# Kernel tuning notes

Measured on AMD Instinct MI355X. Metric: run time of the kernel, lower is better.

Reference implementation:

```python
import jax, jax.numpy as jnp
import numpy as np

H, HD = 8, 32            # num_heads, head_dim
OUT = H * HD             # out_channels = 256
NUM_GRAPHS = 1


def segment_softmax(logits, seg, num_segments):
    m = jax.ops.segment_max(logits, seg, num_segments=num_segments)
    m = jnp.where(jnp.isfinite(m), m, 0.0)
    e = jnp.exp(logits - m[seg])
    s = jax.ops.segment_sum(e, seg, num_segments=num_segments)
    return e / (s[seg] + 1e-16)


def setup_inputs():
    key = jax.random.key(0)
    ks = jax.random.split(key, 16)
    N, E, IN = 30000, 600000, 128
    s = 0.05
    return {
        "x": jax.random.normal(ks[0], (N, IN), jnp.float32),
        "edge_index": jax.random.randint(ks[1], (2, E), 0, N, jnp.int32),
        "edge_attr": jax.random.normal(ks[2], (E,), jnp.float32),
        "batch": jnp.zeros((N,), jnp.int32),
        # per-head GATConv params (stacked over heads)
        "W": jax.random.normal(ks[3], (H, IN, HD), jnp.float32) * s,
        "a_src": jax.random.normal(ks[4], (H, HD), jnp.float32) * s,
        "a_dst": jax.random.normal(ks[5], (H, HD), jnp.float32) * s,
        "conv_b": jnp.zeros((H, HD), jnp.float32),
        # shared fc (used twice in forward)
        "fc_w": jax.random.normal(ks[6], (OUT, OUT), jnp.float32) * s,
        "fc_b": jnp.zeros((OUT,), jnp.float32),
        "ln_w": jnp.ones((OUT,), jnp.float32),
        "ln_b": jnp.zeros((OUT,), jnp.float32),
        "gate_w": jax.random.normal(ks[7], (1, OUT), jnp.float32) * s,
        "gate_b": jnp.zeros((1,), jnp.float32),
        "gfc_w": jax.random.normal(ks[8], (OUT, OUT), jnp.float32) * s,
        "gfc_b": jnp.zeros((OUT,), jnp.float32),
    }


def reference(x, edge_index, edge_attr, batch, W, a_src, a_dst, conv_b,
              fc_w, fc_b, ln_w, ln_b, gate_w, gate_b, gfc_w, gfc_b):
    N = x.shape[0]
    # (dropout p=0.2 is identity in eval mode)
    # --- multi-head GATConv (heads=1 each, vectorized over H); PyG default
    # add_self_loops=True; edge_dim=None so edge_attr is ignored by the conv.
    loops = jnp.arange(N, dtype=edge_index.dtype)
    src = jnp.concatenate([edge_index[0], loops])  # [Etot]
    dst = jnp.concatenate([edge_index[1], loops])
    xp = jnp.einsum('ni,hid->nhd', x, W)                    # [N,H,HD]
    alpha_src = jnp.sum(xp * a_src[None], axis=-1)          # [N,H]
    alpha_dst = jnp.sum(xp * a_dst[None], axis=-1)          # [N,H]
    logits = jax.nn.leaky_relu(alpha_src[src] + alpha_dst[dst], 0.2)  # [Etot,H]
    alpha = segment_softmax(logits, dst, N)                 # [Etot,H]
    msg = alpha[:, :, None] * xp[src]                        # [Etot,H,HD]
    out = jax.ops.segment_sum(msg, dst, num_segments=N) + conv_b[None]
    x_local = out.reshape(N, OUT)                            # concat over heads
    # --- dense re-attention / softmax fusion
    sa = jax.nn.softmax(jax.nn.leaky_relu(x_local @ fc_w.T + fc_b, 0.01), axis=-1)
    x_local = jax.nn.leaky_relu(x_local * sa, 0.2)
    x_local = x_local @ fc_w.T + fc_b
    # LayerNorm (eps=1e-5)
    mu = jnp.mean(x_local, axis=-1, keepdims=True)
    var = jnp.mean(jnp.square(x_local - mu), axis=-1, keepdims=True)
    x_local = (x_local - mu) / jnp.sqrt(var + 1e-5) * ln_w + ln_b
    # F.normalize(p=2, dim=1)
    nrm = jnp.sqrt(jnp.sum(jnp.square(x_local), axis=1, keepdims=True))
    x_local = x_local / jnp.maximum(nrm, 1e-12)
    # --- GlobalAttention pooling
    gate = (x_local @ gate_w.T + gate_b)[:, 0]               # [N]
    g = segment_softmax(gate, batch, NUM_GRAPHS)             # [N]
    x_global = jax.ops.segment_sum(g[:, None] * x_local, batch,
                                   num_segments=NUM_GRAPHS)  # [1,OUT]
    ga = jax.nn.softmax(jax.nn.relu(x_global @ gfc_w.T + gfc_b), axis=-1)
    return x_local * ga[batch]                               # [N,OUT]
```

## Files before the change

kernel.cpp:

```cpp
#include <hip/hip_runtime.h>


#define PAD 96

typedef __attribute__((ext_vector_type(8))) short bf16x8;
typedef __attribute__((ext_vector_type(4))) float f32x4;

__device__ __forceinline__ float leaky_f(float v, float s) { return v > 0.f ? v : s * v; }
__device__ __forceinline__ unsigned short f2bf(float f) {
  unsigned int u = __float_as_uint(f);
  u += 0x7fffu + ((u >> 16) & 1u);
  return (unsigned short)(u >> 16);
}
__device__ __forceinline__ float bf2f(unsigned short u) {
  return __uint_as_float(((unsigned int)u) << 16);
}
__device__ __forceinline__ float red16_sum(float v) {
#pragma unroll
  for (int m = 1; m < 16; m <<= 1) v += __shfl_xor(v, m);
  return v;
}
__device__ __forceinline__ float red16_max(float v) {
#pragma unroll
  for (int m = 1; m < 16; m <<= 1) v = fmaxf(v, __shfl_xor(v, m));
  return v;
}

__global__ void repack_zero_kernel(const float* __restrict__ W, const float* __restrict__ fc_w,
                                   const float* __restrict__ gfc_w,
                                   unsigned short* __restrict__ Wb,
                                   unsigned short* __restrict__ fcB, float* __restrict__ gfcT,
                                   int* __restrict__ count, float* __restrict__ xg,
                                   float* __restrict__ S, int* __restrict__ done, int n) {
  int i = blockIdx.x * 256 + threadIdx.x;
  if (i < 256 * 128) {
    int c = i >> 7, k = i & 127;
    Wb[i] = f2bf(W[((c >> 5) * 128 + k) * 32 + (c & 31)]);
  } else if (i < 256 * 128 + 256 * 256) {
    int j = i - 256 * 128;
    fcB[j] = f2bf(fc_w[j]);
  } else if (i < 256 * 128 + 2 * 256 * 256) {
    int j = i - 256 * 128 - 256 * 256;
    gfcT[j] = gfc_w[(j & 255) * 256 + (j >> 8)];
  }
  if (i < n) count[i] = 0;
  if (i < 256) xg[i] = 0.f;
  if (i == 0) { S[0] = 0.f; done[0] = 0; }
}

template <int A_BF16>
__device__ __forceinline__ void gemm_body_64x256(
    const void* __restrict__ Av, const unsigned short* __restrict__ B,
    int row0, int n_rows, int K, short As[64][72], short Bs[256][72],
    f32x4 acc[4][4]) {
  int t = threadIdx.x;
  int wave = t >> 6, lane = t & 63;
  int m16 = lane & 15, quad = lane >> 4;
  int wc = wave * 64;
  for (int k0 = 0; k0 < K; k0 += 64) {
    if (A_BF16) {
      const unsigned short* A = (const unsigned short*)Av;
#pragma unroll
      for (int p = 0; p < 2; ++p) {
        int e = (p * 256 + t) * 8;
        int row = e >> 6, k = e & 63;
        int ar = row0 + row; if (ar > n_rows - 1) ar = n_rows - 1;
        uint4 q = *(const uint4*)(A + (size_t)ar * K + k0 + k);
        *(uint4*)&As[row][k] = q;
      }
    } else {
      const float* A = (const float*)Av;
#pragma unroll
      for (int p = 0; p < 4; ++p) {
        int e = (p * 256 + t) * 4;
        int row = e >> 6, k = e & 63;
        int ar = row0 + row; if (ar > n_rows - 1) ar = n_rows - 1;
        float4 q = *(const float4*)(A + (size_t)ar * K + k0 + k);
        unsigned int lo = (unsigned int)f2bf(q.x) | ((unsigned int)f2bf(q.y) << 16);
        unsigned int hi = (unsigned int)f2bf(q.z) | ((unsigned int)f2bf(q.w) << 16);
        *(uint2*)&As[row][k] = make_uint2(lo, hi);
      }
    }
#pragma unroll
    for (int p = 0; p < 8; ++p) {
      int e = (p * 256 + t) * 8;
      int nn = e >> 6, k = e & 63;
      uint4 q = *(const uint4*)(B + (size_t)nn * K + k0 + k);
      *(uint4*)&Bs[nn][k] = q;
    }
    __syncthreads();
#pragma unroll
    for (int ks = 0; ks < 64; ks += 32) {
      bf16x8 af[4], bfr[4];
#pragma unroll
      for (int i = 0; i < 4; ++i)
        af[i] = *(const bf16x8*)&As[i * 16 + m16][ks + quad * 8];
#pragma unroll
      for (int j = 0; j < 4; ++j)
        bfr[j] = *(const bf16x8*)&Bs[wc + j * 16 + m16][ks + quad * 8];
#pragma unroll
      for (int i = 0; i < 4; ++i)
#pragma unroll
        for (int j = 0; j < 4; ++j)
          acc[i][j] = __builtin_amdgcn_mfma_f32_16x16x32_bf16(af[i], bfr[j], acc[i][j], 0, 0, 0);
    }
    __syncthreads();
  }
}

__global__ __launch_bounds__(256) void gemm_xp_scatter(
    const float* __restrict__ A, const unsigned short* __restrict__ B,
    const float* __restrict__ a_src, const float* __restrict__ a_dst,
    unsigned short* __restrict__ xpb, float* __restrict__ asrc,
    float* __restrict__ adst, int n_rows,
    const int* __restrict__ esrc, const int* __restrict__ edst,
    int* __restrict__ count, int* __restrict__ ssrc, int E, int gemm_blocks) {
  __shared__ short As[64][72];
  __shared__ short Bs[256][72];
  if ((int)blockIdx.x >= gemm_blocks) {
    int i = ((int)blockIdx.x - gemm_blocks) * 256 + threadIdx.x;
    if (i < E) {
      int d = edst[i];
      int p = atomicAdd(&count[d], 1);
      if (p < PAD) ssrc[(size_t)d * PAD + p] = esrc[i];
    }
    return;
  }
  int t = threadIdx.x;
  int wave = t >> 6, lane = t & 63;
  int m16 = lane & 15, quad = lane >> 4;
  int wc = wave * 64;
  int row0 = blockIdx.x * 64;
  f32x4 acc[4][4];
#pragma unroll
  for (int i = 0; i < 4; ++i)
#pragma unroll
    for (int j = 0; j < 4; ++j) acc[i][j] = (f32x4){0.f, 0.f, 0.f, 0.f};
  gemm_body_64x256<0>(A, B, row0, n_rows, 128, As, Bs, acc);

  float av[4], bd[4];
#pragma unroll
  for (int j = 0; j < 4; ++j) {
    int c = wc + j * 16 + m16;
    av[j] = a_src[c];
    bd[j] = a_dst[c];
  }
#pragma unroll
  for (int i = 0; i < 4; ++i)
#pragma unroll
    for (int v = 0; v < 4; ++v) {
      int r = row0 + i * 16 + quad * 4 + v;
      if (r < n_rows) {
#pragma unroll
        for (int j = 0; j < 4; ++j)
          xpb[(size_t)r * 256 + wc + j * 16 + m16] = f2bf(acc[i][j][v]);
      }
      float s0 = acc[i][0][v] * av[0] + acc[i][1][v] * av[1];
      float s1 = acc[i][2][v] * av[2] + acc[i][3][v] * av[3];
      float d0 = acc[i][0][v] * bd[0] + acc[i][1][v] * bd[1];
      float d1 = acc[i][2][v] * bd[2] + acc[i][3][v] * bd[3];
      s0 = red16_sum(s0); s1 = red16_sum(s1);
      d0 = red16_sum(d0); d1 = red16_sum(d1);
      if (m16 == 0 && r < n_rows) {
        asrc[(size_t)r * 8 + 2 * wave] = s0;
        asrc[(size_t)r * 8 + 2 * wave + 1] = s1;
        adst[(size_t)r * 8 + 2 * wave] = d0;
        adst[(size_t)r * 8 + 2 * wave + 1] = d1;
      }
    }
}

__global__ __launch_bounds__(256) void gemm_sm(
    const float* __restrict__ A, const unsigned short* __restrict__ B,
    const float* __restrict__ bias, unsigned short* __restrict__ x2b, int n_rows) {
  __shared__ short As[64][72];
  __shared__ short Bs[256][72];
  __shared__ float red[4][64];
  __shared__ float rowv[64];
  int t = threadIdx.x;
  int wave = t >> 6, lane = t & 63;
  int m16 = lane & 15, quad = lane >> 4;
  int wc = wave * 64;
  int row0 = blockIdx.x * 64;
  f32x4 acc[4][4];
#pragma unroll
  for (int i = 0; i < 4; ++i)
#pragma unroll
    for (int j = 0; j < 4; ++j) acc[i][j] = (f32x4){0.f, 0.f, 0.f, 0.f};
  gemm_body_64x256<0>(A, B, row0, n_rows, 256, As, Bs, acc);

  float bvv[4];
#pragma unroll
  for (int j = 0; j < 4; ++j) bvv[j] = bias[wc + j * 16 + m16];
#pragma unroll
  for (int i = 0; i < 4; ++i)
#pragma unroll
    for (int j = 0; j < 4; ++j)
#pragma unroll
      for (int v = 0; v < 4; ++v)
        acc[i][j][v] = leaky_f(acc[i][j][v] + bvv[j], 0.01f);

  float M[4][4];
#pragma unroll
  for (int i = 0; i < 4; ++i)
#pragma unroll
    for (int v = 0; v < 4; ++v) {
      float m = fmaxf(fmaxf(acc[i][0][v], acc[i][1][v]), fmaxf(acc[i][2][v], acc[i][3][v]));
      M[i][v] = red16_max(m);
    }
  if (m16 == 0)
#pragma unroll
    for (int i = 0; i < 4; ++i)
#pragma unroll
      for (int v = 0; v < 4; ++v) red[wave][i * 16 + quad * 4 + v] = M[i][v];
  __syncthreads();
  if (t < 64) rowv[t] = fmaxf(fmaxf(red[0][t], red[1][t]), fmaxf(red[2][t], red[3][t]));
  __syncthreads();
#pragma unroll
  for (int i = 0; i < 4; ++i)
#pragma unroll
    for (int v = 0; v < 4; ++v) M[i][v] = rowv[i * 16 + quad * 4 + v];
  __syncthreads();

  float S[4][4];
#pragma unroll
  for (int i = 0; i < 4; ++i)
#pragma unroll
    for (int v = 0; v < 4; ++v) {
#pragma unroll
      for (int j = 0; j < 4; ++j) acc[i][j][v] = __expf(acc[i][j][v] - M[i][v]);
      float s = acc[i][0][v] + acc[i][1][v] + acc[i][2][v] + acc[i][3][v];
      S[i][v] = red16_sum(s);
    }
  if (m16 == 0)
#pragma unroll
    for (int i = 0; i < 4; ++i)
#pragma unroll
      for (int v = 0; v < 4; ++v) red[wave][i * 16 + quad * 4 + v] = S[i][v];
  __syncthreads();
  if (t < 64) rowv[t] = red[0][t] + red[1][t] + red[2][t] + red[3][t];
  __syncthreads();

#pragma unroll
  for (int i = 0; i < 4; ++i)
#pragma unroll
    for (int v = 0; v < 4; ++v) {
      int r = row0 + i * 16 + quad * 4 + v;
      float inv = 1.f / rowv[i * 16 + quad * 4 + v];
      if (r < n_rows) {
#pragma unroll
        for (int j = 0; j < 4; ++j) {
          int c = wc + j * 16 + m16;
          float xv = A[(size_t)r * 256 + c];
          x2b[(size_t)r * 256 + c] = f2bf(leaky_f(xv * acc[i][j][v] * inv, 0.2f));
        }
      }
    }
}

__global__ __launch_bounds__(256) void gemm_ln(
    const unsigned short* __restrict__ A, const unsigned short* __restrict__ B,
    const float* __restrict__ bias, const float* __restrict__ ln_w,
    const float* __restrict__ ln_b, const float* __restrict__ gate_w,
    const float* __restrict__ gate_b, unsigned short* __restrict__ Cout,
    float* __restrict__ egate, int n_rows) {
  __shared__ short As[64][72];
  __shared__ short Bs[256][72];
  __shared__ float red[4][64];
  __shared__ float rowv[64];
  int t = threadIdx.x;
  int wave = t >> 6, lane = t & 63;
  int m16 = lane & 15, quad = lane >> 4;
  int wc = wave * 64;
  int row0 = blockIdx.x * 64;
  f32x4 acc[4][4];
#pragma unroll
  for (int i = 0; i < 4; ++i)
#pragma unroll
    for (int j = 0; j < 4; ++j) acc[i][j] = (f32x4){0.f, 0.f, 0.f, 0.f};
  gemm_body_64x256<1>(A, B, row0, n_rows, 256, As, Bs, acc);

  float bvv[4], lw[4], lb[4], gw[4];
#pragma unroll
  for (int j = 0; j < 4; ++j) {
    int c = wc + j * 16 + m16;
    bvv[j] = bias[c]; lw[j] = ln_w[c]; lb[j] = ln_b[c]; gw[j] = gate_w[c];
  }
#pragma unroll
  for (int i = 0; i < 4; ++i)
#pragma unroll
    for (int j = 0; j < 4; ++j)
#pragma unroll
      for (int v = 0; v < 4; ++v) acc[i][j][v] += bvv[j];

  float MU[4][4];
#pragma unroll
  for (int i = 0; i < 4; ++i)
#pragma unroll
    for (int v = 0; v < 4; ++v)
      MU[i][v] = red16_sum(acc[i][0][v] + acc[i][1][v] + acc[i][2][v] + acc[i][3][v]);
  if (m16 == 0)
#pragma unroll
    for (int i = 0; i < 4; ++i)
#pragma unroll
      for (int v = 0; v < 4; ++v) red[wave][i * 16 + quad * 4 + v] = MU[i][v];
  __syncthreads();
  if (t < 64) rowv[t] = (red[0][t] + red[1][t] + red[2][t] + red[3][t]) * (1.f / 256.f);
  __syncthreads();
#pragma unroll
  for (int i = 0; i < 4; ++i)
#pragma unroll
    for (int v = 0; v < 4; ++v) MU[i][v] = rowv[i * 16 + quad * 4 + v];
  __syncthreads();
#pragma unroll
  for (int i = 0; i < 4; ++i)
#pragma unroll
    for (int j = 0; j < 4; ++j)
#pragma unroll
      for (int v = 0; v < 4; ++v) acc[i][j][v] -= MU[i][v];

  float RS[4][4];
#pragma unroll
  for (int i = 0; i < 4; ++i)
#pragma unroll
    for (int v = 0; v < 4; ++v) {
      float q = acc[i][0][v] * acc[i][0][v] + acc[i][1][v] * acc[i][1][v] +
                acc[i][2][v] * acc[i][2][v] + acc[i][3][v] * acc[i][3][v];
      RS[i][v] = red16_sum(q);
    }
  if (m16 == 0)
#pragma unroll
    for (int i = 0; i < 4; ++i)
#pragma unroll
      for (int v = 0; v < 4; ++v) red[wave][i * 16 + quad * 4 + v] = RS[i][v];
  __syncthreads();
  if (t < 64)
    rowv[t] = rsqrtf((red[0][t] + red[1][t] + red[2][t] + red[3][t]) * (1.f / 256.f) + 1e-5f);
  __syncthreads();
#pragma unroll
  for (int i = 0; i < 4; ++i)
#pragma unroll
    for (int v = 0; v < 4; ++v) RS[i][v] = rowv[i * 16 + quad * 4 + v];
  __syncthreads();
#pragma unroll
  for (int i = 0; i < 4; ++i)
#pragma unroll
    for (int j = 0; j < 4; ++j)
#pragma unroll
      for (int v = 0; v < 4; ++v)
        acc[i][j][v] = acc[i][j][v] * RS[i][v] * lw[j] + lb[j];

  float NV[4][4];
#pragma unroll
  for (int i = 0; i < 4; ++i)
#pragma unroll
    for (int v = 0; v < 4; ++v) {
      float q = acc[i][0][v] * acc[i][0][v] + acc[i][1][v] * acc[i][1][v] +
                acc[i][2][v] * acc[i][2][v] + acc[i][3][v] * acc[i][3][v];
      NV[i][v] = red16_sum(q);
    }
  if (m16 == 0)
#pragma unroll
    for (int i = 0; i < 4; ++i)
#pragma unroll
      for (int v = 0; v < 4; ++v) red[wave][i * 16 + quad * 4 + v] = NV[i][v];
  __syncthreads();
  if (t < 64)
    rowv[t] = 1.f / fmaxf(sqrtf(red[0][t] + red[1][t] + red[2][t] + red[3][t]), 1e-12f);
  __syncthreads();
#pragma unroll
  for (int i = 0; i < 4; ++i)
#pragma unroll
    for (int v = 0; v < 4; ++v) NV[i][v] = rowv[i * 16 + quad * 4 + v];
  __syncthreads();
#pragma unroll
  for (int i = 0; i < 4; ++i)
#pragma unroll
    for (int j = 0; j < 4; ++j)
#pragma unroll
      for (int v = 0; v < 4; ++v) acc[i][j][v] *= NV[i][v];

  float GP[4][4];
#pragma unroll
  for (int i = 0; i < 4; ++i)
#pragma unroll
    for (int v = 0; v < 4; ++v) {
      float g = acc[i][0][v] * gw[0] + acc[i][1][v] * gw[1] +
                acc[i][2][v] * gw[2] + acc[i][3][v] * gw[3];
      GP[i][v] = red16_sum(g);
    }
  if (m16 == 0)
#pragma unroll
    for (int i = 0; i < 4; ++i)
#pragma unroll
      for (int v = 0; v < 4; ++v) red[wave][i * 16 + quad * 4 + v] = GP[i][v];
  __syncthreads();
  if (t < 64 && row0 + t < n_rows) {
    float gp = red[0][t] + red[1][t] + red[2][t] + red[3][t];
    egate[row0 + t] = __expf(gp + gate_b[0]);
  }
#pragma unroll
  for (int i = 0; i < 4; ++i)
#pragma unroll
    for (int v = 0; v < 4; ++v) {
      int r = row0 + i * 16 + quad * 4 + v;
      if (r < n_rows) {
#pragma unroll
        for (int j = 0; j < 4; ++j)
          Cout[(size_t)r * 256 + wc + j * 16 + m16] = f2bf(acc[i][j][v]);
      }
    }
}

__global__ __launch_bounds__(256) void agg_kernel(
    const unsigned short* __restrict__ xpb, const float* __restrict__ asrc,
    const float* __restrict__ adst, const int* __restrict__ count,
    const int* __restrict__ ssrc, const float4* __restrict__ conv_b4,
    float4* __restrict__ xloc4, int n_nodes) {
  int lane = threadIdx.x & 63, w = threadIdx.x >> 6;
  int n = blockIdx.x * 4 + w;
  if (n >= n_nodes) return;
  int h = lane >> 3;
  float ad = adst[n * 8 + h];
  float p = __expf(leaky_f(asrc[n * 8 + h] + ad, 0.2f));
  ushort4 xq = ((const ushort4*)(xpb + (size_t)n * 256))[lane];
  float4 acc;
  acc.x = p * bf2f(xq.x); acc.y = p * bf2f(xq.y);
  acc.z = p * bf2f(xq.z); acc.w = p * bf2f(xq.w);
  float ssum = p;
  int beg = n * PAD;
  int end = beg + count[n];
  int j = beg;
  for (; j + 8 <= end; j += 8) {
    int sv[8];
#pragma unroll
    for (int u = 0; u < 8; ++u) sv[u] = ssrc[j + u];
    float a[8];
#pragma unroll
    for (int u = 0; u < 8; ++u) a[u] = asrc[sv[u] * 8 + h];
    ushort4 q[8];
#pragma unroll
    for (int u = 0; u < 8; ++u) q[u] = ((const ushort4*)(xpb + (size_t)sv[u] * 256))[lane];
#pragma unroll
    for (int u = 0; u < 8; ++u) {
      float pu = __expf(leaky_f(a[u] + ad, 0.2f));
      acc.x += pu * bf2f(q[u].x); acc.y += pu * bf2f(q[u].y);
      acc.z += pu * bf2f(q[u].z); acc.w += pu * bf2f(q[u].w);
      ssum += pu;
    }
  }
  for (; j + 4 <= end; j += 4) {
    int sv0 = ssrc[j], sv1 = ssrc[j + 1], sv2 = ssrc[j + 2], sv3 = ssrc[j + 3];
    float a0 = asrc[sv0 * 8 + h];
    float a1 = asrc[sv1 * 8 + h];
    float a2 = asrc[sv2 * 8 + h];
    float a3 = asrc[sv3 * 8 + h];
    ushort4 q0 = ((const ushort4*)(xpb + (size_t)sv0 * 256))[lane];
    ushort4 q1 = ((const ushort4*)(xpb + (size_t)sv1 * 256))[lane];
    ushort4 q2 = ((const ushort4*)(xpb + (size_t)sv2 * 256))[lane];
    ushort4 q3 = ((const ushort4*)(xpb + (size_t)sv3 * 256))[lane];
    float p0 = __expf(leaky_f(a0 + ad, 0.2f));
    float p1 = __expf(leaky_f(a1 + ad, 0.2f));
    float p2 = __expf(leaky_f(a2 + ad, 0.2f));
    float p3 = __expf(leaky_f(a3 + ad, 0.2f));
    acc.x += p0 * bf2f(q0.x); acc.y += p0 * bf2f(q0.y);
    acc.z += p0 * bf2f(q0.z); acc.w += p0 * bf2f(q0.w);
    acc.x += p1 * bf2f(q1.x); acc.y += p1 * bf2f(q1.y);
    acc.z += p1 * bf2f(q1.z); acc.w += p1 * bf2f(q1.w);
    acc.x += p2 * bf2f(q2.x); acc.y += p2 * bf2f(q2.y);
    acc.z += p2 * bf2f(q2.z); acc.w += p2 * bf2f(q2.w);
    acc.x += p3 * bf2f(q3.x); acc.y += p3 * bf2f(q3.y);
    acc.z += p3 * bf2f(q3.z); acc.w += p3 * bf2f(q3.w);
    ssum += p0 + p1 + p2 + p3;
  }
  for (; j < end; ++j) {
    int sv = ssrc[j];
    float a1 = asrc[sv * 8 + h];
    ushort4 q = ((const ushort4*)(xpb + (size_t)sv * 256))[lane];
    float p1 = __expf(leaky_f(a1 + ad, 0.2f));
    acc.x += p1 * bf2f(q.x); acc.y += p1 * bf2f(q.y);
    acc.z += p1 * bf2f(q.z); acc.w += p1 * bf2f(q.w);
    ssum += p1;
  }
  float inv = 1.f / (ssum + 1e-16f);
  float4 b = conv_b4[lane];
  float4 o;
  o.x = acc.x * inv + b.x; o.y = acc.y * inv + b.y;
  o.z = acc.z * inv + b.z; o.w = acc.w * inv + b.w;
  xloc4[(size_t)n * 64 + lane] = o;
}

__global__ __launch_bounds__(256) void pool_gfc(
    const unsigned short* __restrict__ xlb, const float* __restrict__ egate,
    float* __restrict__ xg, float* __restrict__ Ssum, int n, int* __restrict__ done,
    const float* __restrict__ gfcT, const float* __restrict__ gfc_b,
    float* __restrict__ ga) {
  int c = threadIdx.x;
  int rpb = (n + (int)gridDim.x - 1) / (int)gridDim.x;
  int r0 = blockIdx.x * rpb;
  int r1 = r0 + rpb; if (r1 > n) r1 = n;
  float acc = 0.f, gs = 0.f;
  for (int r = r0; r < r1; ++r) {
    float g = egate[r];
    acc += g * bf2f(xlb[(size_t)r * 256 + c]);
    gs += g;
  }
  atomicAdd(&xg[c], acc);
  if (c == 0) atomicAdd(Ssum, gs);
  __threadfence();
  __shared__ int isLast;
  if (c == 0) {
    int ticket = atomicAdd(done, 1);
    isLast = (ticket == (int)gridDim.x - 1);
  }
  __syncthreads();
  if (!isLast) return;
  __shared__ float xs[256];
  __shared__ float red[256];
  __shared__ float Sv;
  if (c == 0) Sv = atomicAdd(Ssum, 0.f);
  float xgc = atomicAdd(&xg[c], 0.f);
  __syncthreads();
  xs[c] = xgc / (Sv + 1e-16f);
  __syncthreads();
  float a = gfc_b[c];
  for (int i = 0; i < 256; ++i) a += xs[i] * gfcT[i * 256 + c];
  a = fmaxf(a, 0.f);
  red[c] = a;
  __syncthreads();
  for (int s = 128; s > 0; s >>= 1) {
    if (c < s) red[c] = fmaxf(red[c], red[c + s]);
    __syncthreads();
  }
  float m = red[0];
  __syncthreads();
  float e = __expf(a - m);
  red[c] = e;
  __syncthreads();
  for (int s = 128; s > 0; s >>= 1) {
    if (c < s) red[c] += red[c + s];
    __syncthreads();
  }
  ga[c] = e / red[0];
}

__global__ void out_kernel(const ushort4* __restrict__ xlb4, const float4* __restrict__ ga4,
                           float4* __restrict__ out4, int total4) {
  int i = blockIdx.x * 256 + threadIdx.x;
  if (i >= total4) return;
  ushort4 q = xlb4[i];
  float4 g = ga4[i & 63];
  float4 v;
  v.x = bf2f(q.x) * g.x; v.y = bf2f(q.y) * g.y;
  v.z = bf2f(q.z) * g.z; v.w = bf2f(q.w) * g.w;
  out4[i] = v;
}

extern "C" void kernel_launch(void* const* d_in, const int* in_sizes, int n_in,
                              void* d_out, int out_size, void* d_ws, size_t ws_size,
                              hipStream_t stream) {
  const float* x      = (const float*)d_in[0];
  const int* edge_idx = (const int*)d_in[1];
  const float* W      = (const float*)d_in[4];
  const float* a_src  = (const float*)d_in[5];
  const float* a_dst  = (const float*)d_in[6];
  const float* conv_b = (const float*)d_in[7];
  const float* fc_w   = (const float*)d_in[8];
  const float* fc_b   = (const float*)d_in[9];
  const float* ln_w   = (const float*)d_in[10];
  const float* ln_b   = (const float*)d_in[11];
  const float* gate_w = (const float*)d_in[12];
  const float* gate_b = (const float*)d_in[13];
  const float* gfc_w  = (const float*)d_in[14];
  const float* gfc_b  = (const float*)d_in[15];
  (void)n_in; (void)out_size; (void)ws_size;

  int N = in_sizes[0] / 128;
  int E = in_sizes[1] / 2;
  const int* src = edge_idx;
  const int* dst = edge_idx + E;

  char* p = (char*)d_ws;
  auto alloc = [&](size_t bytes) -> char* {
    char* r = p;
    p += (bytes + 255) & ~(size_t)255;
    return r;
  };
  float*          xloc = (float*)alloc((size_t)N * 256 * 4);
  unsigned short* xpb  = (unsigned short*)alloc((size_t)N * 256 * 2);
  unsigned short* x2b  = (unsigned short*)alloc((size_t)N * 256 * 2);
  unsigned short* xlb  = (unsigned short*)alloc((size_t)N * 256 * 2);
  float* asrc  = (float*)alloc((size_t)N * 8 * 4);
  float* adst  = (float*)alloc((size_t)N * 8 * 4);
  unsigned short* Wb   = (unsigned short*)alloc(256 * 128 * 2);
  unsigned short* fcB  = (unsigned short*)alloc(256 * 256 * 2);
  float* gfcT  = (float*)alloc(256 * 256 * 4);
  float* egate = (float*)alloc((size_t)N * 4);
  int*   count = (int*)alloc((size_t)N * 4);
  int*   ssrc  = (int*)alloc((size_t)N * PAD * 4);
  float* Ssum  = (float*)alloc(256);
  int*   done  = (int*)alloc(256);
  float* xg    = (float*)alloc(1024);
  float* ga    = (float*)alloc(1024);

  int eb = (E + 255) / 256;
  int g64 = (N + 63) / 64;

  repack_zero_kernel<<<(256 * 128 + 2 * 256 * 256 + 255) / 256, 256, 0, stream>>>(
      W, fc_w, gfc_w, Wb, fcB, gfcT, count, xg, Ssum, done, N);
  gemm_xp_scatter<<<g64 + eb, 256, 0, stream>>>(
      x, Wb, a_src, a_dst, xpb, asrc, adst, N, src, dst, count, ssrc, E, g64);
  agg_kernel<<<(N + 3) / 4, 256, 0, stream>>>(
      xpb, asrc, adst, count, ssrc, (const float4*)conv_b, (float4*)xloc, N);
  gemm_sm<<<g64, 256, 0, stream>>>(xloc, fcB, fc_b, x2b, N);
  gemm_ln<<<g64, 256, 0, stream>>>(x2b, fcB, fc_b, ln_w, ln_b, gate_w, gate_b,
                                   xlb, egate, N);
  pool_gfc<<<512, 256, 0, stream>>>(xlb, egate, xg, Ssum, N, done, gfcT, gfc_b, ga);
  out_kernel<<<(N * 64 + 255) / 256, 256, 0, stream>>>(
      (const ushort4*)xlb, (const float4*)ga, (float4*)d_out, N * 64);
}
```

Baseline: 300.5 us.

## Fuse global attention pooling into LayerNorm GEMM epilogue with per-block partials

The gate-weighted pooling sum and the gate normaliser are now computed inside the gemm_ln epilogue from register accumulators and written as per-block partials. A single-block finalize kernel reduces the partials and computes the gfc softmax. This removes the full re-read of the bf16 local features, the egate buffer, the global atomics and the ticket-based last-block logic. The trade-offs are a serial single-block reduction over the partials and extra epilogue work in the GEMM.

```diff
diff --git a/kernel.cpp b/kernel.cpp
--- a/kernel.cpp
+++ b/kernel.cpp
@@ -30,8 +30,7 @@
                                    const float* __restrict__ gfc_w,
                                    unsigned short* __restrict__ Wb,
                                    unsigned short* __restrict__ fcB, float* __restrict__ gfcT,
-                                   int* __restrict__ count, float* __restrict__ xg,
-                                   float* __restrict__ S, int* __restrict__ done, int n) {
+                                   int* __restrict__ count, int n) {
   int i = blockIdx.x * 256 + threadIdx.x;
   if (i < 256 * 128) {
     int c = i >> 7, k = i & 127;
@@ -44,8 +43,6 @@
     gfcT[j] = gfc_w[(j & 255) * 256 + (j >> 8)];
   }
   if (i < n) count[i] = 0;
-  if (i < 256) xg[i] = 0.f;
-  if (i == 0) { S[0] = 0.f; done[0] = 0; }
 }
 
 template <int A_BF16>
@@ -263,11 +260,12 @@
     const float* __restrict__ bias, const float* __restrict__ ln_w,
     const float* __restrict__ ln_b, const float* __restrict__ gate_w,
     const float* __restrict__ gate_b, unsigned short* __restrict__ Cout,
-    float* __restrict__ egate, int n_rows) {
+    float* __restrict__ pooled, float* __restrict__ pooledS, int n_rows) {
   __shared__ short As[64][72];
   __shared__ short Bs[256][72];
   __shared__ float red[4][64];
   __shared__ float rowv[64];
+  __shared__ float eg[64];
   int t = threadIdx.x;
   int wave = t >> 6, lane = t & 63;
   int m16 = lane & 15, quad = lane >> 4;
@@ -395,10 +393,35 @@
 #pragma unroll
       for (int v = 0; v < 4; ++v) red[wave][i * 16 + quad * 4 + v] = GP[i][v];
   __syncthreads();
-  if (t < 64 && row0 + t < n_rows) {
+  if (t < 64) {
     float gp = red[0][t] + red[1][t] + red[2][t] + red[3][t];
-    egate[row0 + t] = __expf(gp + gate_b[0]);
-  }
+    float e = (row0 + t < n_rows) ? __expf(gp + gate_b[0]) : 0.f;
+    eg[t] = e;
+#pragma unroll
+    for (int m = 1; m < 64; m <<= 1) e += __shfl_xor(e, m);
+    if (t == 0) pooledS[blockIdx.x] = e;
+  }
+  __syncthreads();
+
+  {
+    float pt[4] = {0.f, 0.f, 0.f, 0.f};
+#pragma unroll
+    for (int i = 0; i < 4; ++i)
+#pragma unroll
+      for (int v = 0; v < 4; ++v) {
+        float w = eg[i * 16 + quad * 4 + v];
+#pragma unroll
+        for (int j = 0; j < 4; ++j) pt[j] += w * acc[i][j][v];
+      }
+#pragma unroll
+    for (int j = 0; j < 4; ++j) {
+      float sj = pt[j];
+      sj += __shfl_xor(sj, 16);
+      sj += __shfl_xor(sj, 32);
+      if (quad == 0) pooled[(size_t)blockIdx.x * 256 + wc + j * 16 + m16] = sj;
+    }
+  }
+
 #pragma unroll
   for (int i = 0; i < 4; ++i)
 #pragma unroll
@@ -490,58 +513,55 @@
   xloc4[(size_t)n * 64 + lane] = o;
 }
 
-__global__ __launch_bounds__(256) void pool_gfc(
-    const unsigned short* __restrict__ xlb, const float* __restrict__ egate,
-    float* __restrict__ xg, float* __restrict__ Ssum, int n, int* __restrict__ done,
+__global__ __launch_bounds__(1024) void finalize_gfc(
+    const float* __restrict__ pooled, const float* __restrict__ pooledS, int nb,
     const float* __restrict__ gfcT, const float* __restrict__ gfc_b,
     float* __restrict__ ga) {
-  int c = threadIdx.x;
-  int rpb = (n + (int)gridDim.x - 1) / (int)gridDim.x;
-  int r0 = blockIdx.x * rpb;
-  int r1 = r0 + rpb; if (r1 > n) r1 = n;
-  float acc = 0.f, gs = 0.f;
-  for (int r = r0; r < r1; ++r) {
-    float g = egate[r];
-    acc += g * bf2f(xlb[(size_t)r * 256 + c]);
-    gs += g;
-  }
-  atomicAdd(&xg[c], acc);
-  if (c == 0) atomicAdd(Ssum, gs);
-  __threadfence();
-  __shared__ int isLast;
-  if (c == 0) {
-    int ticket = atomicAdd(done, 1);
-    isLast = (ticket == (int)gridDim.x - 1);
-  }
-  __syncthreads();
-  if (!isLast) return;
+  __shared__ float sm[1024];
   __shared__ float xs[256];
-  __shared__ float red[256];
-  __shared__ float Sv;
-  if (c == 0) Sv = atomicAdd(Ssum, 0.f);
-  float xgc = atomicAdd(&xg[c], 0.f);
-  __syncthreads();
-  xs[c] = xgc / (Sv + 1e-16f);
-  __syncthreads();
-  float a = gfc_b[c];
-  for (int i = 0; i < 256; ++i) a += xs[i] * gfcT[i * 256 + c];
-  a = fmaxf(a, 0.f);
-  red[c] = a;
-  __syncthreads();
-  for (int s = 128; s > 0; s >>= 1) {
-    if (c < s) red[c] = fmaxf(red[c], red[c + s]);
+  __shared__ float av[256];
+  int t = threadIdx.x, c = t & 255, part = t >> 8;
+  float s = 0.f;
+  for (int b = t; b < nb; b += 1024) s += pooledS[b];
+  sm[t] = s;
+  __syncthreads();
+  for (int st = 512; st > 0; st >>= 1) {
+    if (t < st) sm[t] += sm[t + st];
     __syncthreads();
   }
-  float m = red[0];
-  __syncthreads();
-  float e = __expf(a - m);
-  red[c] = e;
-  __syncthreads();
-  for (int s = 128; s > 0; s >>= 1) {
-    if (c < s) red[c] += red[c + s];
+  float S = sm[0];
+  __syncthreads();
+  float xc = 0.f;
+#pragma unroll 4
+  for (int b = part; b < nb; b += 4) xc += pooled[(size_t)b * 256 + c];
+  sm[t] = xc;
+  __syncthreads();
+  if (part == 0) xs[c] = (sm[c] + sm[c + 256] + sm[c + 512] + sm[c + 768]) / (S + 1e-16f);
+  __syncthreads();
+  float a = 0.f;
+  for (int i = part * 64; i < part * 64 + 64; ++i) a += xs[i] * gfcT[i * 256 + c];
+  sm[t] = a;
+  __syncthreads();
+  if (part == 0)
+    av[c] = fmaxf(sm[c] + sm[c + 256] + sm[c + 512] + sm[c + 768] + gfc_b[c], 0.f);
+  __syncthreads();
+  sm[t] = (t < 256) ? av[t] : -1e30f;
+  __syncthreads();
+  for (int st = 512; st > 0; st >>= 1) {
+    if (t < st) sm[t] = fmaxf(sm[t], sm[t + st]);
     __syncthreads();
   }
-  ga[c] = e / red[0];
+  float m = sm[0];
+  __syncthreads();
+  if (part == 0) av[c] = __expf(av[c] - m);
+  __syncthreads();
+  sm[t] = (t < 256) ? av[t] : 0.f;
+  __syncthreads();
+  for (int st = 512; st > 0; st >>= 1) {
+    if (t < st) sm[t] += sm[t + st];
+    __syncthreads();
+  }
+  if (part == 0) ga[c] = av[c] / sm[0];
 }
 
 __global__ void out_kernel(const ushort4* __restrict__ xlb4, const float4* __restrict__ ga4,
@@ -586,6 +606,7 @@
     p += (bytes + 255) & ~(size_t)255;
     return r;
   };
+  int g64 = (N + 63) / 64;
   float*          xloc = (float*)alloc((size_t)N * 256 * 4);
   unsigned short* xpb  = (unsigned short*)alloc((size_t)N * 256 * 2);
   unsigned short* x2b  = (unsigned short*)alloc((size_t)N * 256 * 2);
@@ -595,27 +616,24 @@
   unsigned short* Wb   = (unsigned short*)alloc(256 * 128 * 2);
   unsigned short* fcB  = (unsigned short*)alloc(256 * 256 * 2);
   float* gfcT  = (float*)alloc(256 * 256 * 4);
-  float* egate = (float*)alloc((size_t)N * 4);
   int*   count = (int*)alloc((size_t)N * 4);
   int*   ssrc  = (int*)alloc((size_t)N * PAD * 4);
-  float* Ssum  = (float*)alloc(256);
-  int*   done  = (int*)alloc(256);
-  float* xg    = (float*)alloc(1024);
+  float* pooled  = (float*)alloc((size_t)g64 * 256 * 4);
+  float* pooledS = (float*)alloc((size_t)g64 * 4);
   float* ga    = (float*)alloc(1024);
 
   int eb = (E + 255) / 256;
-  int g64 = (N + 63) / 64;
 
   repack_zero_kernel<<<(256 * 128 + 2 * 256 * 256 + 255) / 256, 256, 0, stream>>>(
-      W, fc_w, gfc_w, Wb, fcB, gfcT, count, xg, Ssum, done, N);
+      W, fc_w, gfc_w, Wb, fcB, gfcT, count, N);
   gemm_xp_scatter<<<g64 + eb, 256, 0, stream>>>(
       x, Wb, a_src, a_dst, xpb, asrc, adst, N, src, dst, count, ssrc, E, g64);
   agg_kernel<<<(N + 3) / 4, 256, 0, stream>>>(
       xpb, asrc, adst, count, ssrc, (const float4*)conv_b, (float4*)xloc, N);
   gemm_sm<<<g64, 256, 0, stream>>>(xloc, fcB, fc_b, x2b, N);
   gemm_ln<<<g64, 256, 0, stream>>>(x2b, fcB, fc_b, ln_w, ln_b, gate_w, gate_b,
-                                   xlb, egate, N);
-  pool_gfc<<<512, 256, 0, stream>>>(xlb, egate, xg, Ssum, N, done, gfcT, gfc_b, ga);
+                                   xlb, pooled, pooledS, N);
+  finalize_gfc<<<1, 1024, 0, stream>>>(pooled, pooledS, g64, gfcT, gfc_b, ga);
   out_kernel<<<(N * 64 + 255) / 256, 256, 0, stream>>>(
       (const ushort4*)xlb, (const float4*)ga, (float4*)d_out, N * 64);
 }
```

Result: faster. 250.5 us (-16.6%).
